# Kernel tuning notes

Measured on AMD Instinct MI355X. Metric: run time of the kernel, lower is better.

Reference implementation:

```python
import jax, jax.numpy as jnp
import numpy as np

EPS = 1e-5
NEG_SLOPE = 0.01  # torch F.leaky_relu default


def _batchnorm(h, gamma, beta):
    # BatchNorm1d in training mode: batch stats over node dim, biased variance
    mu = jnp.mean(h, axis=0)
    var = jnp.mean((h - mu) ** 2, axis=0)
    return gamma * (h - mu) * jax.lax.rsqrt(var + EPS) + beta


def setup_inputs() -> dict:
    N, E, H, ED = 16384, 524288, 128, 16
    key = jax.random.key(0)
    ks = jax.random.split(key, 12)
    s = 1.0 / np.sqrt(H)
    return {
        "x": jax.random.normal(ks[0], (N, H), jnp.float32),
        "edge_index": jax.random.randint(ks[1], (2, E), 0, N, jnp.int64),
        "edge_attr": jax.random.normal(ks[2], (E, ED), jnp.float32),
        "Wq": jax.random.normal(ks[3], (H, H), jnp.float32) * s,
        "bq": jnp.zeros((H,), jnp.float32),
        "Wk": jax.random.normal(ks[4], (H, H), jnp.float32) * s,
        "bk": jnp.zeros((H,), jnp.float32),
        "Wv": jax.random.normal(ks[5], (H, H), jnp.float32) * s,
        "bv": jnp.zeros((H,), jnp.float32),
        "We": jax.random.normal(ks[6], (ED, 1), jnp.float32) * (1.0 / np.sqrt(ED)),
        "be": jnp.zeros((1,), jnp.float32),
        "bn1_g": jnp.ones((H,), jnp.float32),
        "bn1_b": jnp.zeros((H,), jnp.float32),
        "W1": jax.random.normal(ks[7], (H, 2 * H), jnp.float32) * s,
        "b1": jnp.zeros((2 * H,), jnp.float32),
        "W2": jax.random.normal(ks[8], (2 * H, H), jnp.float32) * (1.0 / np.sqrt(2 * H)),
        "b2": jnp.zeros((H,), jnp.float32),
        "bn2_g": jnp.ones((H,), jnp.float32),
        "bn2_b": jnp.zeros((H,), jnp.float32),
    }


def reference(x, edge_index, edge_attr, Wq, bq, Wk, bk, Wv, bv, We, be,
              bn1_g, bn1_b, W1, b1, W2, b2, bn2_g, bn2_b):
    N = x.shape[0]
    Q = x @ Wq + bq  # [N, H]
    K = x @ Wk + bk
    V = x @ Wv + bv
    Ebias = (edge_attr @ We + be)[:, 0]  # [E], num_heads == 1
    src, dst = edge_index[0], edge_index[1]
    # per-edge dot product over the FULL hidden dim (as in the source)
    scores = jnp.sum(Q[src] * K[dst], axis=1) + Ebias  # [E]
    scores = jnp.where(scores >= 0, scores, NEG_SLOPE * scores)
    # to_dense_adj scatter-adds edge_attr into a dense [N, N] adjacency
    adj = jnp.zeros((N, N), x.dtype).at[src, dst].add(scores)
    attn = jax.nn.softmax(adj, axis=1)  # dense softmax incl. zero non-edges
    x_new = attn @ V  # [N, H]
    h = _batchnorm(x + x_new, bn1_g, bn1_b)
    ffn = jax.nn.relu(h @ W1 + b1) @ W2 + b2
    return _batchnorm(h + ffn, bn2_g, bn2_b)
```

## Files before the change

### kernel.cpp

```cpp
#include <hip/hip_runtime.h>
#include <hip/hip_bf16.h>
#include <math.h>

#define H 128
#define H2 256
#define SLAB 96
#define LDA 136
#define LDA2 264
#define EPS 1e-5f

typedef __attribute__((ext_vector_type(8))) short s16x8;
typedef __attribute__((ext_vector_type(4))) float f32x4;

__device__ __forceinline__ unsigned short f2bf(float f) {
  unsigned u = __float_as_uint(f);
  unsigned r = (u + 0x7FFFu + ((u >> 16) & 1u)) >> 16;
  return (unsigned short)r;
}
__device__ __forceinline__ float bf2f(unsigned short s) {
  return __uint_as_float(((unsigned)s) << 16);
}

__global__ void wprep(const float* __restrict__ Wq, const float* __restrict__ Wk,
                      const float* __restrict__ Wv, const float* __restrict__ W1,
                      const float* __restrict__ W2,
                      short* qh, short* ql, short* kh, short* kl,
                      short* vh, short* w1h, short* w2h)
{
  int job = blockIdx.z;
  const float* src; short* dh; short* dl = nullptr; int Kd, Nn;
  if (job == 0)      { src = Wq; dh = qh;  dl = ql; Kd = 128; Nn = 128; }
  else if (job == 1) { src = Wk; dh = kh;  dl = kl; Kd = 128; Nn = 128; }
  else if (job == 2) { src = Wv; dh = vh;           Kd = 128; Nn = 128; }
  else if (job == 3) { src = W1; dh = w1h;          Kd = 128; Nn = 256; }
  else               { src = W2; dh = w2h;          Kd = 256; Nn = 128; }
  int t = blockIdx.x * 256 + threadIdx.x;
  if (t >= Kd * Nn) return;
  int n = t / Kd, k = t - n * Kd;
  float v = src[(size_t)k * Nn + n];
  unsigned short h = f2bf(v);
  dh[t] = (short)h;
  if (dl) dl[t] = (short)f2bf(v - bf2f(h));
}

__global__ __launch_bounds__(256) void qkv_mfma(
    const float* __restrict__ x,
    const short* __restrict__ Wqh, const short* __restrict__ Wql,
    const short* __restrict__ Wkh, const short* __restrict__ Wkl,
    const short* __restrict__ Wvh,
    const float* __restrict__ bq, const float* __restrict__ bk,
    const float* __restrict__ bv,
    float* __restrict__ Q, unsigned short* __restrict__ Kbf,
    unsigned short* __restrict__ Vbf, float* __restrict__ SVp)
{
  __shared__ __align__(16) short Ahi[64 * LDA];
  __shared__ __align__(16) short Alo[64 * LDA];
  int tid = threadIdx.x;
  int bm = blockIdx.x * 64;
  int wave = tid >> 6, lane = tid & 63;
  int quad = lane >> 4, l16 = lane & 15;
  int wn = wave * 32;

#pragma unroll
  for (int i = 0; i < 4; ++i) {
    int g = i * 256 + tid;
    int row = g >> 4, f = g & 15;
    const float4* xp = (const float4*)&x[(size_t)(bm + row) * H + f * 8];
    float4 v0 = xp[0], v1 = xp[1];
    float vv[8] = {v0.x, v0.y, v0.z, v0.w, v1.x, v1.y, v1.z, v1.w};
    s16x8 hv, lv;
#pragma unroll
    for (int j = 0; j < 8; ++j) {
      unsigned short hh = f2bf(vv[j]);
      hv[j] = (short)hh;
      lv[j] = (short)f2bf(vv[j] - bf2f(hh));
    }
    *(s16x8*)&Ahi[row * LDA + f * 8] = hv;
    *(s16x8*)&Alo[row * LDA + f * 8] = lv;
  }
  __syncthreads();

  for (int ph = 0; ph < 3; ++ph) {
    const short* Bh = (ph == 0) ? Wqh : (ph == 1) ? Wkh : Wvh;
    const short* Bl = (ph == 0) ? Wql : (ph == 1) ? Wkl : nullptr;

    s16x8 bh[2][4], bl2[2][4];
#pragma unroll
    for (int nt = 0; nt < 2; ++nt)
#pragma unroll
      for (int ks = 0; ks < 4; ++ks)
        bh[nt][ks] = *(const s16x8*)&Bh[(size_t)(wn + nt * 16 + l16) * H + ks * 32 + quad * 8];
    if (Bl) {
#pragma unroll
      for (int nt = 0; nt < 2; ++nt)
#pragma unroll
        for (int ks = 0; ks < 4; ++ks)
          bl2[nt][ks] = *(const s16x8*)&Bl[(size_t)(wn + nt * 16 + l16) * H + ks * 32 + quad * 8];
    }

    f32x4 acc[4][2];
#pragma unroll
    for (int mt = 0; mt < 4; ++mt)
#pragma unroll
      for (int nt = 0; nt < 2; ++nt) acc[mt][nt] = (f32x4){0.f, 0.f, 0.f, 0.f};

#pragma unroll
    for (int ks = 0; ks < 4; ++ks) {
      int kof = ks * 32 + quad * 8;
      s16x8 ah[4], al[4];
#pragma unroll
      for (int mt = 0; mt < 4; ++mt) {
        ah[mt] = *(s16x8*)&Ahi[(mt * 16 + l16) * LDA + kof];
        al[mt] = *(s16x8*)&Alo[(mt * 16 + l16) * LDA + kof];
      }
#pragma unroll
      for (int mt = 0; mt < 4; ++mt)
#pragma unroll
        for (int nt = 0; nt < 2; ++nt) {
          acc[mt][nt] = __builtin_amdgcn_mfma_f32_16x16x32_bf16(ah[mt], bh[nt][ks], acc[mt][nt], 0, 0, 0);
          if (ph < 2) {
            acc[mt][nt] = __builtin_amdgcn_mfma_f32_16x16x32_bf16(ah[mt], bl2[nt][ks], acc[mt][nt], 0, 0, 0);
            acc[mt][nt] = __builtin_amdgcn_mfma_f32_16x16x32_bf16(al[mt], bh[nt][ks], acc[mt][nt], 0, 0, 0);
          }
        }
    }

    if (ph == 0) {
#pragma unroll
      for (int nt = 0; nt < 2; ++nt) {
        int col = wn + nt * 16 + l16;
        float bb = bq[col];
#pragma unroll
        for (int mt = 0; mt < 4; ++mt)
#pragma unroll
          for (int r = 0; r < 4; ++r) {
            int row = bm + mt * 16 + quad * 4 + r;
            Q[(size_t)row * H + col] = acc[mt][nt][r] + bb;
          }
      }
    } else if (ph == 1) {
#pragma unroll
      for (int nt = 0; nt < 2; ++nt) {
        int col = wn + nt * 16 + l16;
        float bb = bk[col];
#pragma unroll
        for (int mt = 0; mt < 4; ++mt)
#pragma unroll
          for (int r = 0; r < 4; ++r) {
            int row = bm + mt * 16 + quad * 4 + r;
            Kbf[(size_t)row * H + col] = f2bf(acc[mt][nt][r] + bb);
          }
      }
    } else {
      int bank = blockIdx.x & 7;
#pragma unroll
      for (int nt = 0; nt < 2; ++nt) {
        int col = wn + nt * 16 + l16;
        float bb = bv[col];
        float ps = 0.f;
#pragma unroll
        for (int mt = 0; mt < 4; ++mt)
#pragma unroll
          for (int r = 0; r < 4; ++r) {
            int row = bm + mt * 16 + quad * 4 + r;
            float v = acc[mt][nt][r] + bb;
            Vbf[(size_t)row * H + col] = f2bf(v);
            ps += v;
          }
        ps += __shfl_xor(ps, 16);
        ps += __shfl_xor(ps, 32);
        if (quad == 0) atomicAdd(&SVp[bank * H + col], ps);
      }
    }
  }
}

__global__ void ebfill(const float* __restrict__ ea,
                       const float* __restrict__ We,
                       const float* __restrict__ be,
                       const int* __restrict__ ei,
                       int* __restrict__ cnt,
                       int2* __restrict__ slabDE, int E, int N)
{
  int grp = blockIdx.x & 7;
  int blk = blockIdx.x >> 3;
  int lo = grp * (N >> 3), hi = lo + (N >> 3);
  int per = E >> 8;
  int base = blk * per;
  float4 w0 = *(const float4*)&We[0], w1 = *(const float4*)&We[4];
  float4 w2 = *(const float4*)&We[8], w3 = *(const float4*)&We[12];
  float bias = be[0];
  for (int i = 0; i < per; i += 256) {
    int e = base + i + threadIdx.x;
    if (e >= E) continue;
    int src = ei[e];
    if (src < lo || src >= hi) continue;
    int dst = ei[E + e];
    const float4* p = (const float4*)&ea[(size_t)e * 16];
    float4 a0 = p[0], a1 = p[1], a2 = p[2], a3 = p[3];
    float s = a0.x * w0.x + a0.y * w0.y + a0.z * w0.z + a0.w * w0.w
            + a1.x * w1.x + a1.y * w1.y + a1.z * w1.z + a1.w * w1.w
            + a2.x * w2.x + a2.y * w2.y + a2.z * w2.z + a2.w * w2.w
            + a3.x * w3.x + a3.y * w3.y + a3.z * w3.z + a3.w * w3.w;
    s += bias;
    int pos = atomicAdd(&cnt[src], 1);
    if (pos < SLAB) {
      int2 rec; rec.x = dst; rec.y = __float_as_int(s);
      slabDE[src * SLAB + pos] = rec;
    }
  }
}

__global__ __launch_bounds__(256) void ffn_fused(
    const float* __restrict__ h1, const short* __restrict__ W1h,
    const float* __restrict__ b1, const short* __restrict__ W2h,
    const float* __restrict__ b2,
    const float* __restrict__ sum1p, const float* __restrict__ sq1p,
    const float* __restrict__ g1, const float* __restrict__ bb1,
    float* __restrict__ h2, float* __restrict__ sum2p, float* __restrict__ sq2p,
    float invN)
{
  __shared__ __align__(16) short As[32 * LDA];
  __shared__ __align__(16) short Ts[32 * LDA2];
  __shared__ float aF[H], bF[H];
  int tid = threadIdx.x;
  int bm = blockIdx.x * 32;
  int wave = tid >> 6, lane = tid & 63;
  int quad = lane >> 4, l16 = lane & 15;

  if (tid < H) {
    float s = 0.f, q = 0.f;
#pragma unroll
    for (int b = 0; b < 16; ++b) { s += sum1p[b * H + tid]; q += sq1p[b * H + tid]; }
    float mu = s * invN;
    float var = q * invN - mu * mu;
    float rs = rsqrtf(var + EPS);
    float a = g1[tid] * rs;
    aF[tid] = a;
    bF[tid] = bb1[tid] - a * mu;
  }
  __syncthreads();

  int f = tid & 15;
#pragma unroll
  for (int i = 0; i < 2; ++i) {
    int g = i * 256 + tid;
    int row = g >> 4;
    const float4* xp = (const float4*)&h1[(size_t)(bm + row) * H + f * 8];
    float4 v0 = xp[0], v1 = xp[1];
    float vv[8] = {v0.x, v0.y, v0.z, v0.w, v1.x, v1.y, v1.z, v1.w};
    s16x8 hv;
#pragma unroll
    for (int j = 0; j < 8; ++j) {
      int c = f * 8 + j;
      hv[j] = (short)f2bf(aF[c] * vv[j] + bF[c]);
    }
    *(s16x8*)&As[row * LDA + f * 8] = hv;
  }

  int wn1 = wave * 64;
  s16x8 b1f[4][4];
#pragma unroll
  for (int nt = 0; nt < 4; ++nt)
#pragma unroll
    for (int ks = 0; ks < 4; ++ks)
      b1f[nt][ks] = *(const s16x8*)&W1h[(size_t)(wn1 + nt * 16 + l16) * H + ks * 32 + quad * 8];
  __syncthreads();

  f32x4 acc1[2][4];
#pragma unroll
  for (int mt = 0; mt < 2; ++mt)
#pragma unroll
    for (int nt = 0; nt < 4; ++nt) acc1[mt][nt] = (f32x4){0.f, 0.f, 0.f, 0.f};

#pragma unroll
  for (int ks = 0; ks < 4; ++ks) {
    int kof = ks * 32 + quad * 8;
    s16x8 ah[2];
#pragma unroll
    for (int mt = 0; mt < 2; ++mt) ah[mt] = *(s16x8*)&As[(mt * 16 + l16) * LDA + kof];
#pragma unroll
    for (int mt = 0; mt < 2; ++mt)
#pragma unroll
      for (int nt = 0; nt < 4; ++nt)
        acc1[mt][nt] = __builtin_amdgcn_mfma_f32_16x16x32_bf16(ah[mt], b1f[nt][ks], acc1[mt][nt], 0, 0, 0);
  }

#pragma unroll
  for (int nt = 0; nt < 4; ++nt) {
    int col = wn1 + nt * 16 + l16;
    float bb = b1[col];
#pragma unroll
    for (int mt = 0; mt < 2; ++mt)
#pragma unroll
      for (int r = 0; r < 4; ++r) {
        int row = mt * 16 + quad * 4 + r;
        float v = acc1[mt][nt][r] + bb;
        v = v > 0.f ? v : 0.f;
        Ts[row * LDA2 + col] = (short)f2bf(v);
      }
  }

  int wn2 = wave * 32;
  s16x8 b2f[2][8];
#pragma unroll
  for (int nt = 0; nt < 2; ++nt)
#pragma unroll
    for (int ks = 0; ks < 8; ++ks)
      b2f[nt][ks] = *(const s16x8*)&W2h[(size_t)(wn2 + nt * 16 + l16) * H2 + ks * 32 + quad * 8];
  __syncthreads();

  f32x4 acc2[2][2];
#pragma unroll
  for (int mt = 0; mt < 2; ++mt)
#pragma unroll
    for (int nt = 0; nt < 2; ++nt) acc2[mt][nt] = (f32x4){0.f, 0.f, 0.f, 0.f};

#pragma unroll
  for (int ks = 0; ks < 8; ++ks) {
    int kof = ks * 32 + quad * 8;
    s16x8 ah[2];
#pragma unroll
    for (int mt = 0; mt < 2; ++mt) ah[mt] = *(s16x8*)&Ts[(mt * 16 + l16) * LDA2 + kof];
#pragma unroll
    for (int mt = 0; mt < 2; ++mt)
#pragma unroll
      for (int nt = 0; nt < 2; ++nt)
        acc2[mt][nt] = __builtin_amdgcn_mfma_f32_16x16x32_bf16(ah[mt], b2f[nt][ks], acc2[mt][nt], 0, 0, 0);
  }

  int bank = blockIdx.x & 15;
#pragma unroll
  for (int nt = 0; nt < 2; ++nt) {
    int col = wn2 + nt * 16 + l16;
    float ra = aF[col], rb = bF[col];
    float bb = b2[col];
    float ps = 0.f, pq = 0.f;
#pragma unroll
    for (int mt = 0; mt < 2; ++mt)
#pragma unroll
      for (int r = 0; r < 4; ++r) {
        int row = bm + mt * 16 + quad * 4 + r;
        float rr = ra * h1[(size_t)row * H + col] + rb;
        float v = acc2[mt][nt][r] + bb + rr;
        h2[(size_t)row * H + col] = v;
        ps += v; pq += v * v;
      }
    ps += __shfl_xor(ps, 16); ps += __shfl_xor(ps, 32);
    pq += __shfl_xor(pq, 16); pq += __shfl_xor(pq, 32);
    if (quad == 0) {
      atomicAdd(&sum2p[bank * H + col], ps);
      atomicAdd(&sq2p[bank * H + col], pq);
    }
  }
}

__global__ __launch_bounds__(256) void score_slab(
    const float* __restrict__ Q, const unsigned short* __restrict__ Kbf,
    const int* __restrict__ cnt, const int2* __restrict__ slabDE,
    float* __restrict__ sAslab, int N)
{
  int tid = threadIdx.x;
  int team = tid >> 3, sub = tid & 7;
  int local = team & 15;
  int i = blockIdx.x * 2 + (team >> 4);
  int k = cnt[i]; if (k > SLAB) k = SLAB;
  const float4* q4 = (const float4*)(Q + (size_t)i * H);
  float4 qa0 = q4[2 * sub], qa1 = q4[2 * sub + 1];
  float4 qb0 = q4[16 + 2 * sub], qb1 = q4[17 + 2 * sub];
  int base = i * SLAB;

  for (int p = local * 2; p < k; p += 32) {
    int2 de0 = slabDE[base + p];
    bool has1 = (p + 1 < k);
    int2 de1 = has1 ? slabDE[base + p + 1] : de0;
    const s16x8* k0 = (const s16x8*)(Kbf + (size_t)de0.x * H);
    const s16x8* k1 = (const s16x8*)(Kbf + (size_t)de1.x * H);
    s16x8 ka0 = k0[sub], kb0 = k0[8 + sub];
    s16x8 ka1 = k1[sub], kb1 = k1[8 + sub];
    float p0, p1;
    p0 = qa0.x * bf2f((unsigned short)ka0[0]) + qa0.y * bf2f((unsigned short)ka0[1])
       + qa0.z * bf2f((unsigned short)ka0[2]) + qa0.w * bf2f((unsigned short)ka0[3])
       + qa1.x * bf2f((unsigned short)ka0[4]) + qa1.y * bf2f((unsigned short)ka0[5])
       + qa1.z * bf2f((unsigned short)ka0[6]) + qa1.w * bf2f((unsigned short)ka0[7])
       + qb0.x * bf2f((unsigned short)kb0[0]) + qb0.y * bf2f((unsigned short)kb0[1])
       + qb0.z * bf2f((unsigned short)kb0[2]) + qb0.w * bf2f((unsigned short)kb0[3])
       + qb1.x * bf2f((unsigned short)kb0[4]) + qb1.y * bf2f((unsigned short)kb0[5])
       + qb1.z * bf2f((unsigned short)kb0[6]) + qb1.w * bf2f((unsigned short)kb0[7]);
    p1 = qa0.x * bf2f((unsigned short)ka1[0]) + qa0.y * bf2f((unsigned short)ka1[1])
       + qa0.z * bf2f((unsigned short)ka1[2]) + qa0.w * bf2f((unsigned short)ka1[3])
       + qa1.x * bf2f((unsigned short)ka1[4]) + qa1.y * bf2f((unsigned short)ka1[5])
       + qa1.z * bf2f((unsigned short)ka1[6]) + qa1.w * bf2f((unsigned short)ka1[7])
       + qb0.x * bf2f((unsigned short)kb1[0]) + qb0.y * bf2f((unsigned short)kb1[1])
       + qb0.z * bf2f((unsigned short)kb1[2]) + qb0.w * bf2f((unsigned short)kb1[3])
       + qb1.x * bf2f((unsigned short)kb1[4]) + qb1.y * bf2f((unsigned short)kb1[5])
       + qb1.z * bf2f((unsigned short)kb1[6]) + qb1.w * bf2f((unsigned short)kb1[7]);
    p0 += __shfl_xor(p0, 1); p1 += __shfl_xor(p1, 1);
    p0 += __shfl_xor(p0, 2); p1 += __shfl_xor(p1, 2);
    p0 += __shfl_xor(p0, 4); p1 += __shfl_xor(p1, 4);
    if (sub == 0) {
      float s0 = p0 + __int_as_float(de0.y);
      sAslab[base + p] = (s0 >= 0.f) ? s0 : 0.01f * s0;
      if (has1) {
        float s1 = p1 + __int_as_float(de1.y);
        sAslab[base + p + 1] = (s1 >= 0.f) ? s1 : 0.01f * s1;
      }
    }
  }
}

__global__ __launch_bounds__(256) void row_slab(
    const float* __restrict__ x, const unsigned short* __restrict__ Vbf,
    const float* __restrict__ SVp, const int* __restrict__ cnt,
    const float* __restrict__ sAslab, const int2* __restrict__ slabDE,
    float* __restrict__ h1, float* __restrict__ sum1p, float* __restrict__ sq1p,
    int N)
{
  __shared__ float sv[8][SLAB];
  __shared__ int sd[8][SLAB];
  __shared__ unsigned char sown[8][SLAB];
  __shared__ float csum[H], csq[H], svf[H];
  int tid = threadIdx.x;
  int team = tid >> 5, lane = tid & 31;
  int i = blockIdx.x * 8 + team;
  int k = cnt[i]; if (k > SLAB) k = SLAB;
  int base = i * SLAB;

  if (tid < H) {
    csum[tid] = 0.f; csq[tid] = 0.f;
    float s = 0.f;
#pragma unroll
    for (int b = 0; b < 8; ++b) s += SVp[b * H + tid];
    svf[tid] = s;
  }

  for (int p = lane; p < k; p += 32) {
    sv[team][p] = sAslab[base + p];
    sd[team][p] = slabDE[base + p].x;
  }
  __syncthreads();

  for (int p = lane; p < k; p += 32) {
    int d = sd[team][p], o = p;
    for (int q = 0; q < p; ++q)
      if (sd[team][q] == d) { o = q; break; }
    sown[team][p] = (unsigned char)o;
  }
  __syncthreads();
  for (int p = lane; p < k; p += 32)
    if (sown[team][p] != (unsigned char)p)
      atomicAdd(&sv[team][sown[team][p]], sv[team][p]);
  __syncthreads();

  float m = 0.f;
  for (int p = lane; p < k; p += 32)
    if (sown[team][p] == (unsigned char)p) m = fmaxf(m, sv[team][p]);
#pragma unroll
  for (int mask = 16; mask; mask >>= 1) m = fmaxf(m, __shfl_xor(m, mask));
  float em = expf(-m);

  float zl = 0.f;
  for (int p = lane; p < k; p += 32) {
    float cf = 0.f;
    if (sown[team][p] == (unsigned char)p) cf = expf(sv[team][p] - m) - em;
    sv[team][p] = cf;
    zl += cf;
  }
#pragma unroll
  for (int mask = 16; mask; mask >>= 1) zl += __shfl_xor(zl, mask);
  float Zi = 1.f / ((float)N * em + zl);
  __syncthreads();

  const ushort4* V4 = (const ushort4*)Vbf;
  float4 s4 = *(const float4*)&svf[lane * 4];
  float ax = em * s4.x, ay = em * s4.y, az = em * s4.z, aw = em * s4.w;
  int c = 0;
  for (; c + 8 <= k; c += 8) {
    float cf[8]; int dd[8]; ushort4 vv[8];
#pragma unroll
    for (int u = 0; u < 8; ++u) { cf[u] = sv[team][c + u]; dd[u] = sd[team][c + u]; }
#pragma unroll
    for (int u = 0; u < 8; ++u) vv[u] = V4[(size_t)dd[u] * 32 + lane];
#pragma unroll
    for (int u = 0; u < 8; ++u) {
      ax += cf[u] * bf2f(vv[u].x);
      ay += cf[u] * bf2f(vv[u].y);
      az += cf[u] * bf2f(vv[u].z);
      aw += cf[u] * bf2f(vv[u].w);
    }
  }
  for (; c < k; ++c) {
    float cf = sv[team][c];
    ushort4 v0 = V4[(size_t)sd[team][c] * 32 + lane];
    ax += cf * bf2f(v0.x); ay += cf * bf2f(v0.y);
    az += cf * bf2f(v0.z); aw += cf * bf2f(v0.w);
  }
  float4 xx = *(const float4*)&x[(size_t)i * H + lane * 4];
  float4 out;
  out.x = xx.x + ax * Zi; out.y = xx.y + ay * Zi;
  out.z = xx.z + az * Zi; out.w = xx.w + aw * Zi;
  *(float4*)&h1[(size_t)i * H + lane * 4] = out;

  int c0 = lane * 4;
  atomicAdd(&csum[c0 + 0], out.x); atomicAdd(&csq[c0 + 0], out.x * out.x);
  atomicAdd(&csum[c0 + 1], out.y); atomicAdd(&csq[c0 + 1], out.y * out.y);
  atomicAdd(&csum[c0 + 2], out.z); atomicAdd(&csq[c0 + 2], out.z * out.z);
  atomicAdd(&csum[c0 + 3], out.w); atomicAdd(&csq[c0 + 3], out.w * out.w);
  __syncthreads();
  if (tid < H) {
    int bank = blockIdx.x & 15;
    atomicAdd(&sum1p[bank * H + tid], csum[tid]);
    atomicAdd(&sq1p[bank * H + tid], csq[tid]);
  }
}

__global__ __launch_bounds__(256) void bn_apply(
    const float* __restrict__ X,
    const float* __restrict__ sum2p, const float* __restrict__ sq2p,
    const float* __restrict__ g2, const float* __restrict__ bb2,
    float* __restrict__ Y, size_t n4, float invN)
{
  __shared__ float A2s[H], B2s[H];
  int tid = threadIdx.x;
  if (tid < H) {
    float s = 0.f, q = 0.f;
#pragma unroll
    for (int b = 0; b < 16; ++b) { s += sum2p[b * H + tid]; q += sq2p[b * H + tid]; }
    float mu = s * invN;
    float var = q * invN - mu * mu;
    float rs = rsqrtf(var + EPS);
    float a = g2[tid] * rs;
    A2s[tid] = a;
    B2s[tid] = bb2[tid] - a * mu;
  }
  __syncthreads();
  size_t i = (size_t)blockIdx.x * blockDim.x + tid;
  if (i >= n4) return;
  float4 v = ((const float4*)X)[i];
  int c = (int)((i * 4) & (H - 1));
  float4 a = *(const float4*)&A2s[c];
  float4 b = *(const float4*)&B2s[c];
  v.x = a.x * v.x + b.x; v.y = a.y * v.y + b.y;
  v.z = a.z * v.z + b.z; v.w = a.w * v.w + b.w;
  ((float4*)Y)[i] = v;
}

extern "C" void kernel_launch(void* const* d_in, const int* in_sizes, int n_in,
                              void* d_out, int out_size, void* d_ws, size_t ws_size,
                              hipStream_t stream)
{
  const float* x  = (const float*)d_in[0];
  const int*   ei = (const int*)d_in[1];
  const float* ea = (const float*)d_in[2];
  const float* Wq = (const float*)d_in[3];
  const float* bq = (const float*)d_in[4];
  const float* Wk = (const float*)d_in[5];
  const float* bk = (const float*)d_in[6];
  const float* Wv = (const float*)d_in[7];
  const float* bv = (const float*)d_in[8];
  const float* We = (const float*)d_in[9];
  const float* be = (const float*)d_in[10];
  const float* g1 = (const float*)d_in[11];
  const float* bb1 = (const float*)d_in[12];
  const float* W1 = (const float*)d_in[13];
  const float* b1 = (const float*)d_in[14];
  const float* W2 = (const float*)d_in[15];
  const float* b2 = (const float*)d_in[16];
  const float* g2 = (const float*)d_in[17];
  const float* bb2 = (const float*)d_in[18];

  int N = in_sizes[0] / H;
  int E = in_sizes[2] / 16;
  size_t NH = (size_t)N * H;
  float invN = 1.0f / (float)N;

  float* Q   = (float*)d_ws;
  float* KmSlot = Q + NH;
  float* h1  = KmSlot + NH;
  unsigned short* Vbf = (unsigned short*)(h1 + NH);
  int2*  slabDE = (int2*)(Vbf + NH);
  float* sAslab = (float*)(slabDE + (size_t)N * SLAB);
  int*   cnt    = (int*)(sAslab + (size_t)N * SLAB);
  float* stats  = (float*)(cnt + N);
  float* SVp   = stats;
  float* sum1p = stats + 8 * H;
  float* sq1p  = sum1p + 16 * H;
  float* sum2p = sq1p + 16 * H;
  float* sq2p  = sum2p + 16 * H;
  float* statsEnd = sq2p + 16 * H;
  short* wbuf = (short*)statsEnd;
  short* Wqh = wbuf;
  short* Wql = Wqh + 16384;
  short* Wkh = Wql + 16384;
  short* Wkl = Wkh + 16384;
  short* Wvh = Wkl + 16384;
  short* W1h = Wvh + 16384;
  short* W2h = W1h + 32768;
  unsigned short* Kbf = (unsigned short*)KmSlot;
  float* h2 = KmSlot;

  hipMemsetAsync(cnt, 0, (size_t)N * sizeof(int), stream);
  hipMemsetAsync(stats, 0, (size_t)72 * H * sizeof(float), stream);

  wprep<<<dim3(128, 1, 5), 256, 0, stream>>>(Wq, Wk, Wv, W1, W2,
      Wqh, Wql, Wkh, Wkl, Wvh, W1h, W2h);

  qkv_mfma<<<dim3(N / 64), 256, 0, stream>>>(
      x, Wqh, Wql, Wkh, Wkl, Wvh, bq, bk, bv, Q, Kbf, Vbf, SVp);

  ebfill<<<dim3(2048), 256, 0, stream>>>(ea, We, be, ei, cnt, slabDE, E, N);
  score_slab<<<dim3(N / 2), 256, 0, stream>>>(Q, Kbf, cnt, slabDE, sAslab, N);
  row_slab<<<dim3(N / 8), 256, 0, stream>>>(x, Vbf, SVp, cnt, sAslab, slabDE,
                                            h1, sum1p, sq1p, N);

  ffn_fused<<<dim3(N / 32), 256, 0, stream>>>(h1, W1h, b1, W2h, b2,
      sum1p, sq1p, g1, bb1, h2, sum2p, sq2p, invN);

  bn_apply<<<dim3((int)((NH / 4 + 255) / 256)), 256, 0, stream>>>(
      h2, sum2p, sq2p, g2, bb2, (float*)d_out, NH / 4, invN);
}
```

Baseline: 239.4 us.

## Fuse edge score computation into row softmax/aggregation kernel

Merges score_slab and row_slab into a single attn_fused kernel. Each 32-lane team now computes its row's Q·K dot products, keeping leaky-ReLU scores in shared memory, then does dedup, softmax and V aggregation in place. This drops the global sAslab write and read-back, one kernel launch, and several block-wide barriers. In exchange, each row gets only 32 threads for the K gathers instead of 128, so there is less memory-level parallelism per row in the score phase. The code also now relies on in-wave ordering of shared-memory accesses instead of __syncthreads.

```diff
diff --git a/kernel.cpp b/kernel.cpp
--- a/kernel.cpp
+++ b/kernel.cpp
@@ -211,6 +211,152 @@
   }
 }
 
+__global__ __launch_bounds__(256) void attn_fused(
+    const float* __restrict__ x, const float* __restrict__ Q,
+    const unsigned short* __restrict__ Kbf, const unsigned short* __restrict__ Vbf,
+    const float* __restrict__ SVp, const int* __restrict__ cnt,
+    const int2* __restrict__ slabDE,
+    float* __restrict__ h1, float* __restrict__ sum1p, float* __restrict__ sq1p,
+    int N)
+{
+  __shared__ float sv[8][SLAB];
+  __shared__ int sd[8][SLAB];
+  __shared__ unsigned char sown[8][SLAB];
+  __shared__ float csum[H], csq[H], svf[H];
+  int tid = threadIdx.x;
+  int team = tid >> 5, lane = tid & 31;
+  int i = blockIdx.x * 8 + team;
+  int k = cnt[i]; if (k > SLAB) k = SLAB;
+  int base = i * SLAB;
+
+  if (tid < H) {
+    csum[tid] = 0.f; csq[tid] = 0.f;
+    float s = 0.f;
+#pragma unroll
+    for (int b = 0; b < 8; ++b) s += SVp[b * H + tid];
+    svf[tid] = s;
+  }
+
+  for (int p = lane; p < k; p += 32) {
+    int2 de = slabDE[base + p];
+    sd[team][p] = de.x;
+    sv[team][p] = __int_as_float(de.y);
+  }
+  __syncthreads();
+
+  int sub8 = lane & 7, sub4 = lane >> 3;
+  const float4* q4 = (const float4*)(Q + (size_t)i * H);
+  float4 qa0 = q4[2 * sub8], qa1 = q4[2 * sub8 + 1];
+  float4 qb0 = q4[16 + 2 * sub8], qb1 = q4[17 + 2 * sub8];
+  for (int p0 = sub4 * 2; p0 < k; p0 += 8) {
+    int d0 = sd[team][p0];
+    bool has1 = (p0 + 1 < k);
+    int d1 = has1 ? sd[team][p0 + 1] : d0;
+    const s16x8* k0 = (const s16x8*)(Kbf + (size_t)d0 * H);
+    const s16x8* k1 = (const s16x8*)(Kbf + (size_t)d1 * H);
+    s16x8 ka0 = k0[sub8], kb0 = k0[8 + sub8];
+    s16x8 ka1 = k1[sub8], kb1 = k1[8 + sub8];
+    float p0_, p1_;
+    p0_ = qa0.x * bf2f((unsigned short)ka0[0]) + qa0.y * bf2f((unsigned short)ka0[1])
+        + qa0.z * bf2f((unsigned short)ka0[2]) + qa0.w * bf2f((unsigned short)ka0[3])
+        + qa1.x * bf2f((unsigned short)ka0[4]) + qa1.y * bf2f((unsigned short)ka0[5])
+        + qa1.z * bf2f((unsigned short)ka0[6]) + qa1.w * bf2f((unsigned short)ka0[7])
+        + qb0.x * bf2f((unsigned short)kb0[0]) + qb0.y * bf2f((unsigned short)kb0[1])
+        + qb0.z * bf2f((unsigned short)kb0[2]) + qb0.w * bf2f((unsigned short)kb0[3])
+        + qb1.x * bf2f((unsigned short)kb0[4]) + qb1.y * bf2f((unsigned short)kb0[5])
+        + qb1.z * bf2f((unsigned short)kb0[6]) + qb1.w * bf2f((unsigned short)kb0[7]);
+    p1_ = qa0.x * bf2f((unsigned short)ka1[0]) + qa0.y * bf2f((unsigned short)ka1[1])
+        + qa0.z * bf2f((unsigned short)ka1[2]) + qa0.w * bf2f((unsigned short)ka1[3])
+        + qa1.x * bf2f((unsigned short)ka1[4]) + qa1.y * bf2f((unsigned short)ka1[5])
+        + qa1.z * bf2f((unsigned short)ka1[6]) + qa1.w * bf2f((unsigned short)ka1[7])
+        + qb0.x * bf2f((unsigned short)kb1[0]) + qb0.y * bf2f((unsigned short)kb1[1])
+        + qb0.z * bf2f((unsigned short)kb1[2]) + qb0.w * bf2f((unsigned short)kb1[3])
+        + qb1.x * bf2f((unsigned short)kb1[4]) + qb1.y * bf2f((unsigned short)kb1[5])
+        + qb1.z * bf2f((unsigned short)kb1[6]) + qb1.w * bf2f((unsigned short)kb1[7]);
+    p0_ += __shfl_xor(p0_, 1); p1_ += __shfl_xor(p1_, 1);
+    p0_ += __shfl_xor(p0_, 2); p1_ += __shfl_xor(p1_, 2);
+    p0_ += __shfl_xor(p0_, 4); p1_ += __shfl_xor(p1_, 4);
+    if (sub8 == 0) {
+      float s0 = p0_ + sv[team][p0];
+      sv[team][p0] = (s0 >= 0.f) ? s0 : 0.01f * s0;
+      if (has1) {
+        float s1 = p1_ + sv[team][p0 + 1];
+        sv[team][p0 + 1] = (s1 >= 0.f) ? s1 : 0.01f * s1;
+      }
+    }
+  }
+
+  for (int p = lane; p < k; p += 32) {
+    int d = sd[team][p], o = p;
+    for (int q = 0; q < p; ++q)
+      if (sd[team][q] == d) { o = q; break; }
+    sown[team][p] = (unsigned char)o;
+  }
+  for (int p = lane; p < k; p += 32)
+    if (sown[team][p] != (unsigned char)p)
+      atomicAdd(&sv[team][sown[team][p]], sv[team][p]);
+
+  float m = 0.f;
+  for (int p = lane; p < k; p += 32)
+    if (sown[team][p] == (unsigned char)p) m = fmaxf(m, sv[team][p]);
+#pragma unroll
+  for (int mask = 16; mask; mask >>= 1) m = fmaxf(m, __shfl_xor(m, mask));
+  float em = expf(-m);
+
+  float zl = 0.f;
+  for (int p = lane; p < k; p += 32) {
+    float cf = 0.f;
+    if (sown[team][p] == (unsigned char)p) cf = expf(sv[team][p] - m) - em;
+    sv[team][p] = cf;
+    zl += cf;
+  }
+#pragma unroll
+  for (int mask = 16; mask; mask >>= 1) zl += __shfl_xor(zl, mask);
+  float Zi = 1.f / ((float)N * em + zl);
+
+  const ushort4* V4 = (const ushort4*)Vbf;
+  float4 s4 = *(const float4*)&svf[lane * 4];
+  float ax = em * s4.x, ay = em * s4.y, az = em * s4.z, aw = em * s4.w;
+  int c = 0;
+  for (; c + 8 <= k; c += 8) {
+    float cf[8]; int dd[8]; ushort4 vv[8];
+#pragma unroll
+    for (int u = 0; u < 8; ++u) { cf[u] = sv[team][c + u]; dd[u] = sd[team][c + u]; }
+#pragma unroll
+    for (int u = 0; u < 8; ++u) vv[u] = V4[(size_t)dd[u] * 32 + lane];
+#pragma unroll
+    for (int u = 0; u < 8; ++u) {
+      ax += cf[u] * bf2f(vv[u].x);
+      ay += cf[u] * bf2f(vv[u].y);
+      az += cf[u] * bf2f(vv[u].z);
+      aw += cf[u] * bf2f(vv[u].w);
+    }
+  }
+  for (; c < k; ++c) {
+    float cf = sv[team][c];
+    ushort4 v0 = V4[(size_t)sd[team][c] * 32 + lane];
+    ax += cf * bf2f(v0.x); ay += cf * bf2f(v0.y);
+    az += cf * bf2f(v0.z); aw += cf * bf2f(v0.w);
+  }
+  float4 xx = *(const float4*)&x[(size_t)i * H + lane * 4];
+  float4 out;
+  out.x = xx.x + ax * Zi; out.y = xx.y + ay * Zi;
+  out.z = xx.z + az * Zi; out.w = xx.w + aw * Zi;
+  *(float4*)&h1[(size_t)i * H + lane * 4] = out;
+
+  int c0 = lane * 4;
+  atomicAdd(&csum[c0 + 0], out.x); atomicAdd(&csq[c0 + 0], out.x * out.x);
+  atomicAdd(&csum[c0 + 1], out.y); atomicAdd(&csq[c0 + 1], out.y * out.y);
+  atomicAdd(&csum[c0 + 2], out.z); atomicAdd(&csq[c0 + 2], out.z * out.z);
+  atomicAdd(&csum[c0 + 3], out.w); atomicAdd(&csq[c0 + 3], out.w * out.w);
+  __syncthreads();
+  if (tid < H) {
+    int bank = blockIdx.x & 15;
+    atomicAdd(&sum1p[bank * H + tid], csum[tid]);
+    atomicAdd(&sq1p[bank * H + tid], csq[tid]);
+  }
+}
+
 __global__ __launch_bounds__(256) void ffn_fused(
     const float* __restrict__ h1, const short* __restrict__ W1h,
     const float* __restrict__ b1, const short* __restrict__ W2h,
@@ -352,165 +498,6 @@
       atomicAdd(&sum2p[bank * H + col], ps);
       atomicAdd(&sq2p[bank * H + col], pq);
     }
-  }
-}
-
-__global__ __launch_bounds__(256) void score_slab(
-    const float* __restrict__ Q, const unsigned short* __restrict__ Kbf,
-    const int* __restrict__ cnt, const int2* __restrict__ slabDE,
-    float* __restrict__ sAslab, int N)
-{
-  int tid = threadIdx.x;
-  int team = tid >> 3, sub = tid & 7;
-  int local = team & 15;
-  int i = blockIdx.x * 2 + (team >> 4);
-  int k = cnt[i]; if (k > SLAB) k = SLAB;
-  const float4* q4 = (const float4*)(Q + (size_t)i * H);
-  float4 qa0 = q4[2 * sub], qa1 = q4[2 * sub + 1];
-  float4 qb0 = q4[16 + 2 * sub], qb1 = q4[17 + 2 * sub];
-  int base = i * SLAB;
-
-  for (int p = local * 2; p < k; p += 32) {
-    int2 de0 = slabDE[base + p];
-    bool has1 = (p + 1 < k);
-    int2 de1 = has1 ? slabDE[base + p + 1] : de0;
-    const s16x8* k0 = (const s16x8*)(Kbf + (size_t)de0.x * H);
-    const s16x8* k1 = (const s16x8*)(Kbf + (size_t)de1.x * H);
-    s16x8 ka0 = k0[sub], kb0 = k0[8 + sub];
-    s16x8 ka1 = k1[sub], kb1 = k1[8 + sub];
-    float p0, p1;
-    p0 = qa0.x * bf2f((unsigned short)ka0[0]) + qa0.y * bf2f((unsigned short)ka0[1])
-       + qa0.z * bf2f((unsigned short)ka0[2]) + qa0.w * bf2f((unsigned short)ka0[3])
-       + qa1.x * bf2f((unsigned short)ka0[4]) + qa1.y * bf2f((unsigned short)ka0[5])
-       + qa1.z * bf2f((unsigned short)ka0[6]) + qa1.w * bf2f((unsigned short)ka0[7])
-       + qb0.x * bf2f((unsigned short)kb0[0]) + qb0.y * bf2f((unsigned short)kb0[1])
-       + qb0.z * bf2f((unsigned short)kb0[2]) + qb0.w * bf2f((unsigned short)kb0[3])
-       + qb1.x * bf2f((unsigned short)kb0[4]) + qb1.y * bf2f((unsigned short)kb0[5])
-       + qb1.z * bf2f((unsigned short)kb0[6]) + qb1.w * bf2f((unsigned short)kb0[7]);
-    p1 = qa0.x * bf2f((unsigned short)ka1[0]) + qa0.y * bf2f((unsigned short)ka1[1])
-       + qa0.z * bf2f((unsigned short)ka1[2]) + qa0.w * bf2f((unsigned short)ka1[3])
-       + qa1.x * bf2f((unsigned short)ka1[4]) + qa1.y * bf2f((unsigned short)ka1[5])
-       + qa1.z * bf2f((unsigned short)ka1[6]) + qa1.w * bf2f((unsigned short)ka1[7])
-       + qb0.x * bf2f((unsigned short)kb1[0]) + qb0.y * bf2f((unsigned short)kb1[1])
-       + qb0.z * bf2f((unsigned short)kb1[2]) + qb0.w * bf2f((unsigned short)kb1[3])
-       + qb1.x * bf2f((unsigned short)kb1[4]) + qb1.y * bf2f((unsigned short)kb1[5])
-       + qb1.z * bf2f((unsigned short)kb1[6]) + qb1.w * bf2f((unsigned short)kb1[7]);
-    p0 += __shfl_xor(p0, 1); p1 += __shfl_xor(p1, 1);
-    p0 += __shfl_xor(p0, 2); p1 += __shfl_xor(p1, 2);
-    p0 += __shfl_xor(p0, 4); p1 += __shfl_xor(p1, 4);
-    if (sub == 0) {
-      float s0 = p0 + __int_as_float(de0.y);
-      sAslab[base + p] = (s0 >= 0.f) ? s0 : 0.01f * s0;
-      if (has1) {
-        float s1 = p1 + __int_as_float(de1.y);
-        sAslab[base + p + 1] = (s1 >= 0.f) ? s1 : 0.01f * s1;
-      }
-    }
-  }
-}
-
-__global__ __launch_bounds__(256) void row_slab(
-    const float* __restrict__ x, const unsigned short* __restrict__ Vbf,
-    const float* __restrict__ SVp, const int* __restrict__ cnt,
-    const float* __restrict__ sAslab, const int2* __restrict__ slabDE,
-    float* __restrict__ h1, float* __restrict__ sum1p, float* __restrict__ sq1p,
-    int N)
-{
-  __shared__ float sv[8][SLAB];
-  __shared__ int sd[8][SLAB];
-  __shared__ unsigned char sown[8][SLAB];
-  __shared__ float csum[H], csq[H], svf[H];
-  int tid = threadIdx.x;
-  int team = tid >> 5, lane = tid & 31;
-  int i = blockIdx.x * 8 + team;
-  int k = cnt[i]; if (k > SLAB) k = SLAB;
-  int base = i * SLAB;
-
-  if (tid < H) {
-    csum[tid] = 0.f; csq[tid] = 0.f;
-    float s = 0.f;
-#pragma unroll
-    for (int b = 0; b < 8; ++b) s += SVp[b * H + tid];
-    svf[tid] = s;
-  }
-
-  for (int p = lane; p < k; p += 32) {
-    sv[team][p] = sAslab[base + p];
-    sd[team][p] = slabDE[base + p].x;
-  }
-  __syncthreads();
-
-  for (int p = lane; p < k; p += 32) {
-    int d = sd[team][p], o = p;
-    for (int q = 0; q < p; ++q)
-      if (sd[team][q] == d) { o = q; break; }
-    sown[team][p] = (unsigned char)o;
-  }
-  __syncthreads();
-  for (int p = lane; p < k; p += 32)
-    if (sown[team][p] != (unsigned char)p)
-      atomicAdd(&sv[team][sown[team][p]], sv[team][p]);
-  __syncthreads();
-
-  float m = 0.f;
-  for (int p = lane; p < k; p += 32)
-    if (sown[team][p] == (unsigned char)p) m = fmaxf(m, sv[team][p]);
-#pragma unroll
-  for (int mask = 16; mask; mask >>= 1) m = fmaxf(m, __shfl_xor(m, mask));
-  float em = expf(-m);
-
-  float zl = 0.f;
-  for (int p = lane; p < k; p += 32) {
-    float cf = 0.f;
-    if (sown[team][p] == (unsigned char)p) cf = expf(sv[team][p] - m) - em;
-    sv[team][p] = cf;
-    zl += cf;
-  }
-#pragma unroll
-  for (int mask = 16; mask; mask >>= 1) zl += __shfl_xor(zl, mask);
-  float Zi = 1.f / ((float)N * em + zl);
-  __syncthreads();
-
-  const ushort4* V4 = (const ushort4*)Vbf;
-  float4 s4 = *(const float4*)&svf[lane * 4];
-  float ax = em * s4.x, ay = em * s4.y, az = em * s4.z, aw = em * s4.w;
-  int c = 0;
-  for (; c + 8 <= k; c += 8) {
-    float cf[8]; int dd[8]; ushort4 vv[8];
-#pragma unroll
-    for (int u = 0; u < 8; ++u) { cf[u] = sv[team][c + u]; dd[u] = sd[team][c + u]; }
-#pragma unroll
-    for (int u = 0; u < 8; ++u) vv[u] = V4[(size_t)dd[u] * 32 + lane];
-#pragma unroll
-    for (int u = 0; u < 8; ++u) {
-      ax += cf[u] * bf2f(vv[u].x);
-      ay += cf[u] * bf2f(vv[u].y);
-      az += cf[u] * bf2f(vv[u].z);
-      aw += cf[u] * bf2f(vv[u].w);
-    }
-  }
-  for (; c < k; ++c) {
-    float cf = sv[team][c];
-    ushort4 v0 = V4[(size_t)sd[team][c] * 32 + lane];
-    ax += cf * bf2f(v0.x); ay += cf * bf2f(v0.y);
-    az += cf * bf2f(v0.z); aw += cf * bf2f(v0.w);
-  }
-  float4 xx = *(const float4*)&x[(size_t)i * H + lane * 4];
-  float4 out;
-  out.x = xx.x + ax * Zi; out.y = xx.y + ay * Zi;
-  out.z = xx.z + az * Zi; out.w = xx.w + aw * Zi;
-  *(float4*)&h1[(size_t)i * H + lane * 4] = out;
-
-  int c0 = lane * 4;
-  atomicAdd(&csum[c0 + 0], out.x); atomicAdd(&csq[c0 + 0], out.x * out.x);
-  atomicAdd(&csum[c0 + 1], out.y); atomicAdd(&csq[c0 + 1], out.y * out.y);
-  atomicAdd(&csum[c0 + 2], out.z); atomicAdd(&csq[c0 + 2], out.z * out.z);
-  atomicAdd(&csum[c0 + 3], out.w); atomicAdd(&csq[c0 + 3], out.w * out.w);
-  __syncthreads();
-  if (tid < H) {
-    int bank = blockIdx.x & 15;
-    atomicAdd(&sum1p[bank * H + tid], csum[tid]);
-    atomicAdd(&sq1p[bank * H + tid], csq[tid]);
   }
 }
 
@@ -609,9 +596,9 @@
       x, Wqh, Wql, Wkh, Wkl, Wvh, bq, bk, bv, Q, Kbf, Vbf, SVp);
 
   ebfill<<<dim3(2048), 256, 0, stream>>>(ea, We, be, ei, cnt, slabDE, E, N);
-  score_slab<<<dim3(N / 2), 256, 0, stream>>>(Q, Kbf, cnt, slabDE, sAslab, N);
-  row_slab<<<dim3(N / 8), 256, 0, stream>>>(x, Vbf, SVp, cnt, sAslab, slabDE,
-                                            h1, sum1p, sq1p, N);
+
+  attn_fused<<<dim3(N / 8), 256, 0, stream>>>(x, Q, Kbf, Vbf, SVp, cnt, slabDE,
+                                              h1, sum1p, sq1p, N);
 
   ffn_fused<<<dim3(N / 32), 256, 0, stream>>>(h1, W1h, b1, W2h, b2,
       sum1p, sq1p, g1, bb1, h2, sum2p, sq2p, invN);
```

Measured after the change: 226.9 us. 5.2% less time.
